# Performance work log

Measured on AMD Instinct MI355X. Metric: run time of the kernel, lower is better.

The kernel has to match this reference:

```python
import jax, jax.numpy as jnp
import numpy as np

NEG_FILL = -1000.0

def setup_inputs() -> dict:
    key = jax.random.key(0)
    k1, k2, k3, k4 = jax.random.split(key, 4)
    B, N, D = 16, 2048, 64
    q = jax.random.normal(k1, (B, N, D), dtype=jnp.float32)
    k = jax.random.normal(k2, (B, N, D), dtype=jnp.float32)
    v = jax.random.normal(k3, (B, N, D), dtype=jnp.float32)
    mask = jax.random.randint(k4, (B, N, N), 0, 2) == 1
    return {"q": q, "k": k, "v": v, "mask": mask}

def reference(q, k, v, mask):
    # Faithful to the torch module: scale by sqrt(seq_len) = len(q[0])**0.5,
    # masked positions set to -1000.0, softmax over dim=1 (NOT the last dim).
    seq_len = q.shape[1]
    scores = jnp.einsum('bnd,bmd->bnm', q, k) / jnp.sqrt(jnp.float32(seq_len))
    scores = jnp.where(mask, NEG_FILL, scores)
    attn = jax.nn.softmax(scores, axis=1)  # dim=1 as in nn.Softmax(dim=1)
    out = jnp.einsum('bnm,bmd->bnd', attn, v)
    return out
```

## Files before the change

kernel.cpp:

```cpp
#include <hip/hip_runtime.h>
#include <hip/hip_bf16.h>


#define B_ 16
#define N_ 2048
#define D_ 64
#define SCALE 0.022097086912079608f
#define NCH 8

typedef __attribute__((ext_vector_type(8))) short bf16x8;
typedef __attribute__((ext_vector_type(4))) float f32x4;

static __device__ __forceinline__ short f2bf(float x) {
  unsigned u = __float_as_uint(x);
  return (short)((u + 0x7FFF + ((u >> 16) & 1)) >> 16);
}

static __device__ __forceinline__ bf16x8 load8(const short* p) {
  return *reinterpret_cast<const bf16x8*>(p);
}

static __device__ __forceinline__ bf16x8 load8f(const float* p) {
  const f32x4 a = *reinterpret_cast<const f32x4*>(p);
  const f32x4 b = *reinterpret_cast<const f32x4*>(p + 4);
  bf16x8 r;
  r[0] = f2bf(a[0]); r[1] = f2bf(a[1]); r[2] = f2bf(a[2]); r[3] = f2bf(a[3]);
  r[4] = f2bf(b[0]); r[5] = f2bf(b[1]); r[6] = f2bf(b[2]); r[7] = f2bf(b[3]);
  return r;
}

__global__ __launch_bounds__(256) void cvt_bf16(const float* __restrict__ q,
                                                const float* __restrict__ k,
                                                short* __restrict__ qb,
                                                short* __restrict__ kb) {
  const size_t i = ((size_t)blockIdx.x * 256 + threadIdx.x) * 8;
  const float* src = blockIdx.y ? k : q;
  short* dst = blockIdx.y ? kb : qb;
  *reinterpret_cast<bf16x8*>(dst + i) = load8f(src + i);
}

__global__ __launch_bounds__(256) void score_kernel(
    const short* __restrict__ qb, const short* __restrict__ kb,
    const int* __restrict__ mask, short* __restrict__ pstore,
    float* __restrict__ csp) {
  const int b = blockIdx.x;
  const int wave = threadIdx.x >> 6;
  const int lane = threadIdx.x & 63;
  const int l15 = lane & 15;
  const int lhi = lane >> 4;
  const int m0 = blockIdx.y * 128 + wave * 32;
  const int mi = m0 >> 5;
  const int nbase = blockIdx.z * (N_ / NCH);

  const short* qbb = qb + (size_t)b * N_ * D_;
  const short* kbb = kb + (size_t)b * N_ * D_;
  const int* maskb = mask + (size_t)b * N_ * N_;

  bf16x8 kf[2][2];
#pragma unroll
  for (int cg = 0; cg < 2; ++cg) {
    kf[cg][0] = load8(kbb + (m0 + cg * 16 + l15) * D_ + lhi * 8);
    kf[cg][1] = load8(kbb + (m0 + cg * 16 + l15) * D_ + 32 + lhi * 8);
  }

  __shared__ __align__(16) short pbuf[4][16][40];

  float cs0 = 0.f, cs1 = 0.f;

  for (int n0 = nbase; n0 < nbase + N_ / NCH; n0 += 16) {
    int mk[2][4];
#pragma unroll
    for (int cg = 0; cg < 2; ++cg)
#pragma unroll
      for (int r = 0; r < 4; ++r)
        mk[cg][r] =
            maskb[(size_t)(n0 + lhi * 4 + r) * N_ + m0 + cg * 16 + l15];
    const bf16x8 qf0 = load8(qbb + (n0 + l15) * D_ + lhi * 8);
    const bf16x8 qf1 = load8(qbb + (n0 + l15) * D_ + 32 + lhi * 8);
#pragma unroll
    for (int cg = 0; cg < 2; ++cg) {
      f32x4 acc = {0.f, 0.f, 0.f, 0.f};
      acc = __builtin_amdgcn_mfma_f32_16x16x32_bf16(qf0, kf[cg][0], acc, 0, 0, 0);
      acc = __builtin_amdgcn_mfma_f32_16x16x32_bf16(qf1, kf[cg][1], acc, 0, 0, 0);
      float cp = 0.f;
#pragma unroll
      for (int r = 0; r < 4; ++r) {
        const float p = mk[cg][r] ? 0.f : __expf(acc[r] * SCALE);
        cp += p;
        pbuf[wave][lhi * 4 + r][cg * 16 + l15] = f2bf(p);
      }
      if (cg == 0) cs0 += cp; else cs1 += cp;
    }
    __builtin_amdgcn_wave_barrier();
    const bf16x8 pa =
        *reinterpret_cast<const bf16x8*>(&pbuf[wave][l15][lhi * 8]);
    const int n16 = n0 >> 4;
    *reinterpret_cast<bf16x8*>(
        pstore + (((size_t)b * 128 + n16) * 64 + mi) * 512 + lane * 8) = pa;
    __builtin_amdgcn_wave_barrier();
  }

  cs0 += __shfl_xor(cs0, 16, 64);
  cs0 += __shfl_xor(cs0, 32, 64);
  cs1 += __shfl_xor(cs1, 16, 64);
  cs1 += __shfl_xor(cs1, 32, 64);
  float* cspz = csp + ((size_t)b * NCH + blockIdx.z) * N_;
  if (lane < 16) {
    cspz[m0 + l15] = cs0;
    cspz[m0 + 16 + l15] = cs1;
  }
}

__global__ __launch_bounds__(256) void vprep_kernel(
    const float* __restrict__ v, const float* __restrict__ csp,
    short* __restrict__ vt) {
  const int b = blockIdx.x;
  const int m0 = blockIdx.y * 64;
  const int tid = threadIdx.x;
  __shared__ float csl[4][64];
  __shared__ float cst[64];
  __shared__ float lds[64][65];

  {
    const int col = m0 + (tid & 63);
    const int q4 = tid >> 6;
    float s = 0.f;
#pragma unroll
    for (int j = 0; j < 2; ++j)
      s += csp[((size_t)b * NCH + q4 * 2 + j) * N_ + col];
    csl[q4][tid & 63] = s;
  }
  __syncthreads();
  if (tid < 64) cst[tid] = csl[0][tid] + csl[1][tid] + csl[2][tid] + csl[3][tid];
  __syncthreads();

  const float* vb = v + (size_t)b * N_ * D_;
#pragma unroll
  for (int pass = 0; pass < 4; ++pass) {
    const int mloc = pass * 16 + (tid >> 4);
    const int d4 = (tid & 15) * 4;
    const f32x4 x = *reinterpret_cast<const f32x4*>(vb + (m0 + mloc) * D_ + d4);
    const float ic = 1.0f / cst[mloc];
    lds[mloc][d4 + 0] = x[0] * ic;
    lds[mloc][d4 + 1] = x[1] * ic;
    lds[mloc][d4 + 2] = x[2] * ic;
    lds[mloc][d4 + 3] = x[3] * ic;
  }
  __syncthreads();
  const int d = tid >> 2;
  const int seg = tid & 3;
  bf16x8 o0, o1;
#pragma unroll
  for (int i = 0; i < 8; ++i) o0[i] = f2bf(lds[seg * 16 + i][d]);
#pragma unroll
  for (int i = 0; i < 8; ++i) o1[i] = f2bf(lds[seg * 16 + 8 + i][d]);
  short* dst = vt + (size_t)b * D_ * N_ + (size_t)d * N_ + m0 + seg * 16;
  *reinterpret_cast<bf16x8*>(dst) = o0;
  *reinterpret_cast<bf16x8*>(dst + 8) = o1;
}

__global__ __launch_bounds__(256) void pv_kernel(const short* __restrict__ pstore,
                                                 const short* __restrict__ vt,
                                                 float* __restrict__ out) {
  const int b = blockIdx.x;
  const int wave = threadIdx.x >> 6;
  const int lane = threadIdx.x & 63;
  const int l15 = lane & 15;
  const int lhi = lane >> 4;
  const int n0 = blockIdx.y * 64 + wave * 16;
  const int n16 = blockIdx.y * 4 + wave;

  const short* psb =
      pstore + (((size_t)b * 128 + n16) * 64) * 512 + (size_t)lane * 8;
  const short* vtb = vt + (size_t)b * D_ * N_;

  f32x4 oacc[4];
#pragma unroll
  for (int d = 0; d < 4; ++d) oacc[d] = (f32x4){0.f, 0.f, 0.f, 0.f};

#pragma unroll 2
  for (int mi = 0; mi < 64; ++mi) {
    const bf16x8 pa = load8(psb + (size_t)mi * 512);
    const int m0 = mi * 32;
#pragma unroll
    for (int dsub = 0; dsub < 4; ++dsub) {
      const bf16x8 vf =
          load8(vtb + (size_t)(dsub * 16 + l15) * N_ + m0 + lhi * 8);
      oacc[dsub] =
          __builtin_amdgcn_mfma_f32_16x16x32_bf16(pa, vf, oacc[dsub], 0, 0, 0);
    }
  }

  float* dst = out + (size_t)b * N_ * D_;
#pragma unroll
  for (int dsub = 0; dsub < 4; ++dsub)
#pragma unroll
    for (int r = 0; r < 4; ++r)
      dst[(size_t)(n0 + lhi * 4 + r) * D_ + dsub * 16 + l15] = oacc[dsub][r];
}

__global__ __launch_bounds__(256) void colsum_fb(
    const float* __restrict__ q, const float* __restrict__ k,
    const int* __restrict__ mask, float* __restrict__ colsum) {
  const int b = blockIdx.x;
  const int wave = threadIdx.x >> 6;
  const int lane = threadIdx.x & 63;
  const int l15 = lane & 15;
  const int lhi = lane >> 4;
  const int m0 = blockIdx.y * 64 + wave * 16;
  const float* qbp = q + (size_t)b * N_ * D_;
  const float* kbp = k + (size_t)b * N_ * D_;
  const int* maskb = mask + (size_t)b * N_ * N_;
  const bf16x8 kf0 = load8f(kbp + (m0 + l15) * D_ + lhi * 8);
  const bf16x8 kf1 = load8f(kbp + (m0 + l15) * D_ + 32 + lhi * 8);
  float partial = 0.f;
  for (int n0 = 0; n0 < N_; n0 += 16) {
    bf16x8 qf0 = load8f(qbp + (n0 + l15) * D_ + lhi * 8);
    bf16x8 qf1 = load8f(qbp + (n0 + l15) * D_ + 32 + lhi * 8);
    f32x4 acc = {0.f, 0.f, 0.f, 0.f};
    acc = __builtin_amdgcn_mfma_f32_16x16x32_bf16(qf0, kf0, acc, 0, 0, 0);
    acc = __builtin_amdgcn_mfma_f32_16x16x32_bf16(qf1, kf1, acc, 0, 0, 0);
#pragma unroll
    for (int r = 0; r < 4; ++r) {
      const int n = n0 + lhi * 4 + r;
      partial +=
          maskb[(size_t)n * N_ + m0 + l15] ? 0.f : __expf(acc[r] * SCALE);
    }
  }
  partial += __shfl_xor(partial, 16, 64);
  partial += __shfl_xor(partial, 32, 64);
  if (lane < 16) colsum[(size_t)b * N_ + m0 + l15] = partial;
}

__global__ __launch_bounds__(256) void attn_out_fb(
    const float* __restrict__ q, const float* __restrict__ k,
    const float* __restrict__ v, const int* __restrict__ mask,
    const float* __restrict__ colsum, float* __restrict__ out) {
  const int b = blockIdx.x;
  const int wave = threadIdx.x >> 6;
  const int lane = threadIdx.x & 63;
  const int l15 = lane & 15;
  const int lhi = lane >> 4;
  const int n0 = blockIdx.y * 64 + wave * 16;
  const float* qbp = q + (size_t)b * N_ * D_;
  const float* kbp = k + (size_t)b * N_ * D_;
  const float* vbp = v + (size_t)b * N_ * D_;
  const int* maskb = mask + (size_t)b * N_ * N_;
  const float* csb = colsum + (size_t)b * N_;
  const bf16x8 qf0 = load8f(qbp + (n0 + l15) * D_ + lhi * 8);
  const bf16x8 qf1 = load8f(qbp + (n0 + l15) * D_ + 32 + lhi * 8);
  __shared__ __align__(16) short pbuf[4][16][32];
  f32x4 oacc[4];
#pragma unroll
  for (int d = 0; d < 4; ++d) oacc[d] = (f32x4){0.f, 0.f, 0.f, 0.f};
  for (int m0 = 0; m0 < N_; m0 += 32) {
#pragma unroll
    for (int cg = 0; cg < 2; ++cg) {
      const int mc = m0 + cg * 16;
      bf16x8 kf0 = load8f(kbp + (mc + l15) * D_ + lhi * 8);
      bf16x8 kf1 = load8f(kbp + (mc + l15) * D_ + 32 + lhi * 8);
      f32x4 acc = {0.f, 0.f, 0.f, 0.f};
      acc = __builtin_amdgcn_mfma_f32_16x16x32_bf16(qf0, kf0, acc, 0, 0, 0);
      acc = __builtin_amdgcn_mfma_f32_16x16x32_bf16(qf1, kf1, acc, 0, 0, 0);
      const float ic = 1.0f / csb[mc + l15];
#pragma unroll
      for (int r = 0; r < 4; ++r) {
        const int n = n0 + lhi * 4 + r;
        const float p = maskb[(size_t)n * N_ + mc + l15]
                            ? 0.f
                            : __expf(acc[r] * SCALE) * ic;
        pbuf[wave][lhi * 4 + r][cg * 16 + l15] = f2bf(p);
      }
    }
    __syncthreads();
    const bf16x8 pa =
        *reinterpret_cast<const bf16x8*>(&pbuf[wave][l15][lhi * 8]);
#pragma unroll
    for (int dsub = 0; dsub < 4; ++dsub) {
      bf16x8 vf;
#pragma unroll
      for (int j = 0; j < 8; ++j)
        vf[j] = f2bf(vbp[(m0 + lhi * 8 + j) * D_ + dsub * 16 + l15]);
      oacc[dsub] =
          __builtin_amdgcn_mfma_f32_16x16x32_bf16(pa, vf, oacc[dsub], 0, 0, 0);
    }
    __syncthreads();
  }
#pragma unroll
  for (int dsub = 0; dsub < 4; ++dsub)
#pragma unroll
    for (int r = 0; r < 4; ++r)
      out[(size_t)b * N_ * D_ + (size_t)(n0 + lhi * 4 + r) * D_ + dsub * 16 +
          l15] = oacc[dsub][r];
}

extern "C" void kernel_launch(void* const* d_in, const int* in_sizes, int n_in,
                              void* d_out, int out_size, void* d_ws,
                              size_t ws_size, hipStream_t stream) {
  const float* q = (const float*)d_in[0];
  const float* k = (const float*)d_in[1];
  const float* v = (const float*)d_in[2];
  const int* mask = (const int*)d_in[3];
  float* out = (float*)d_out;

  const size_t MB = 1024 * 1024;
  const size_t qb_off = 0;
  const size_t kb_off = qb_off + 4 * MB;
  const size_t vt_off = kb_off + 4 * MB;
  const size_t cs_off = vt_off + 4 * MB;
  const size_t ps_off = cs_off + 1 * MB;
  const size_t need = ps_off + 128 * MB;

  if (ws_size >= need) {
    short* qbf = (short*)((char*)d_ws + qb_off);
    short* kbf = (short*)((char*)d_ws + kb_off);
    short* vt = (short*)((char*)d_ws + vt_off);
    float* csp = (float*)((char*)d_ws + cs_off);
    short* pstore = (short*)((char*)d_ws + ps_off);

    cvt_bf16<<<dim3((B_ * N_ * D_) / (256 * 8), 2), 256, 0, stream>>>(
        q, k, qbf, kbf);
    score_kernel<<<dim3(B_, N_ / 128, NCH), 256, 0, stream>>>(qbf, kbf, mask,
                                                              pstore, csp);
    vprep_kernel<<<dim3(B_, N_ / 64), 256, 0, stream>>>(v, csp, vt);
    pv_kernel<<<dim3(B_, N_ / 64), 256, 0, stream>>>(pstore, vt, out);
  } else {
    float* colsum = (float*)d_ws;
    colsum_fb<<<dim3(B_, N_ / 64), 256, 0, stream>>>(q, k, mask, colsum);
    attn_out_fb<<<dim3(B_, N_ / 64), 256, 0, stream>>>(q, k, v, mask, colsum,
                                                       out);
  }
}
```

Baseline: 461.3 us.

## Split PV reduction across blocks with atomics and prefetch mask in score kernel

Measured after the change: 478.8 us. 1.04x slower.

```diff
diff --git a/kernel.cpp b/kernel.cpp
--- a/kernel.cpp
+++ b/kernel.cpp
@@ -7,6 +7,7 @@
 #define D_ 64
 #define SCALE 0.022097086912079608f
 #define NCH 8
+#define MSPLIT 4
 
 typedef __attribute__((ext_vector_type(8))) short bf16x8;
 typedef __attribute__((ext_vector_type(4))) float f32x4;
@@ -51,11 +52,20 @@
   const int m0 = blockIdx.y * 128 + wave * 32;
   const int mi = m0 >> 5;
   const int nbase = blockIdx.z * (N_ / NCH);
+  const int nend = nbase + N_ / NCH;
 
   const short* qbb = qb + (size_t)b * N_ * D_;
   const short* kbb = kb + (size_t)b * N_ * D_;
   const int* maskb = mask + (size_t)b * N_ * N_;
 
+  int mk[2][4];
+#pragma unroll
+  for (int cg = 0; cg < 2; ++cg)
+#pragma unroll
+    for (int r = 0; r < 4; ++r)
+      mk[cg][r] =
+          maskb[(size_t)(nbase + lhi * 4 + r) * N_ + m0 + cg * 16 + l15];
+
   bf16x8 kf[2][2];
 #pragma unroll
   for (int cg = 0; cg < 2; ++cg) {
@@ -67,14 +77,17 @@
 
   float cs0 = 0.f, cs1 = 0.f;
 
-  for (int n0 = nbase; n0 < nbase + N_ / NCH; n0 += 16) {
-    int mk[2][4];
-#pragma unroll
-    for (int cg = 0; cg < 2; ++cg)
-#pragma unroll
-      for (int r = 0; r < 4; ++r)
-        mk[cg][r] =
-            maskb[(size_t)(n0 + lhi * 4 + r) * N_ + m0 + cg * 16 + l15];
+  for (int n0 = nbase; n0 < nend; n0 += 16) {
+    const int nn = n0 + 16;
+    int mkn[2][4];
+    if (nn < nend) {
+#pragma unroll
+      for (int cg = 0; cg < 2; ++cg)
+#pragma unroll
+        for (int r = 0; r < 4; ++r)
+          mkn[cg][r] =
+              maskb[(size_t)(nn + lhi * 4 + r) * N_ + m0 + cg * 16 + l15];
+    }
     const bf16x8 qf0 = load8(qbb + (n0 + l15) * D_ + lhi * 8);
     const bf16x8 qf1 = load8(qbb + (n0 + l15) * D_ + 32 + lhi * 8);
 #pragma unroll
@@ -98,6 +111,12 @@
     *reinterpret_cast<bf16x8*>(
         pstore + (((size_t)b * 128 + n16) * 64 + mi) * 512 + lane * 8) = pa;
     __builtin_amdgcn_wave_barrier();
+    if (nn < nend) {
+#pragma unroll
+      for (int cg = 0; cg < 2; ++cg)
+#pragma unroll
+        for (int r = 0; r < 4; ++r) mk[cg][r] = mkn[cg][r];
+    }
   }
 
   cs0 += __shfl_xor(cs0, 16, 64);
@@ -169,9 +188,10 @@
   const int lhi = lane >> 4;
   const int n0 = blockIdx.y * 64 + wave * 16;
   const int n16 = blockIdx.y * 4 + wave;
+  const int mi0 = blockIdx.z * (64 / MSPLIT);
 
   const short* psb =
-      pstore + (((size_t)b * 128 + n16) * 64) * 512 + (size_t)lane * 8;
+      pstore + (((size_t)b * 128 + n16) * 64 + mi0) * 512 + (size_t)lane * 8;
   const short* vtb = vt + (size_t)b * D_ * N_;
 
   f32x4 oacc[4];
@@ -179,9 +199,9 @@
   for (int d = 0; d < 4; ++d) oacc[d] = (f32x4){0.f, 0.f, 0.f, 0.f};
 
 #pragma unroll 2
-  for (int mi = 0; mi < 64; ++mi) {
+  for (int mi = 0; mi < 64 / MSPLIT; ++mi) {
     const bf16x8 pa = load8(psb + (size_t)mi * 512);
-    const int m0 = mi * 32;
+    const int m0 = (mi0 + mi) * 32;
 #pragma unroll
     for (int dsub = 0; dsub < 4; ++dsub) {
       const bf16x8 vf =
@@ -196,7 +216,8 @@
   for (int dsub = 0; dsub < 4; ++dsub)
 #pragma unroll
     for (int r = 0; r < 4; ++r)
-      dst[(size_t)(n0 + lhi * 4 + r) * D_ + dsub * 16 + l15] = oacc[dsub][r];
+      unsafeAtomicAdd(&dst[(size_t)(n0 + lhi * 4 + r) * D_ + dsub * 16 + l15],
+                      oacc[dsub][r]);
 }
 
 __global__ __launch_bounds__(256) void colsum_fb(
@@ -318,12 +339,13 @@
     float* csp = (float*)((char*)d_ws + cs_off);
     short* pstore = (short*)((char*)d_ws + ps_off);
 
+    hipMemsetAsync(out, 0, (size_t)B_ * N_ * D_ * sizeof(float), stream);
     cvt_bf16<<<dim3((B_ * N_ * D_) / (256 * 8), 2), 256, 0, stream>>>(
         q, k, qbf, kbf);
     score_kernel<<<dim3(B_, N_ / 128, NCH), 256, 0, stream>>>(qbf, kbf, mask,
                                                               pstore, csp);
     vprep_kernel<<<dim3(B_, N_ / 64), 256, 0, stream>>>(v, csp, vt);
-    pv_kernel<<<dim3(B_, N_ / 64), 256, 0, stream>>>(pstore, vt, out);
+    pv_kernel<<<dim3(B_, N_ / 64, MSPLIT), 256, 0, stream>>>(pstore, vt, out);
   } else {
     float* colsum = (float*)d_ws;
     colsum_fb<<<dim3(B_, N_ / 64), 256, 0, stream>>>(q, k, mask, colsum);
```
